# Optimization experiments

Measured on AMD Instinct MI355X. Metric: run time of the kernel, lower is better.

Reference implementation:

```python
import jax, jax.numpy as jnp
import numpy as np
import math

B, S, D = 4, 2048, 1024
H = 16
HD = D // H  # 64
NEG_INF = -1e9


def setup_inputs() -> dict:
    key = jax.random.key(0)
    k1, k2, k3, k4, k5 = jax.random.split(key, 5)
    x = jax.random.normal(k1, (B, S, D), dtype=jnp.float32)
    # rotary frequencies (theta = 10000), shape (S, HD//2)
    inv_freq = 1.0 / (10000.0 ** (jnp.arange(0, HD, 2, dtype=jnp.float32) / HD))
    t = jnp.arange(S, dtype=jnp.float32)
    freqs = jnp.outer(t, inv_freq)  # (S, HD//2)
    freqs_cos = jnp.cos(freqs)
    freqs_sin = jnp.sin(freqs)
    # causal additive mask (1,1,S,S)
    causal = jnp.tril(jnp.ones((S, S), dtype=bool))
    mask = jnp.where(causal, 0.0, NEG_INF).astype(jnp.float32)[None, None]
    scale = 0.02
    wq = jax.random.normal(k2, (D, D), dtype=jnp.float32) * scale
    wk = jax.random.normal(k3, (D, D), dtype=jnp.float32) * scale
    wv = jax.random.normal(k4, (D, D), dtype=jnp.float32) * scale
    wo = jax.random.normal(k5, (D, D), dtype=jnp.float32) * scale
    return {"x": x, "freqs_cos": freqs_cos, "freqs_sin": freqs_sin,
            "mask": mask, "wq": wq, "wk": wk, "wv": wv, "wo": wo}


def _apply_rotary(t, cos, sin):
    # t: (B,S,H,HD); cos/sin: (S, HD//2) broadcast as (1,S,1,HD//2)
    tr = t.reshape(*t.shape[:-1], HD // 2, 2)
    t0, t1 = tr[..., 0], tr[..., 1]
    c = cos[None, :, None, :]
    s = sin[None, :, None, :]
    o0 = t0 * c - t1 * s
    o1 = t0 * s + t1 * c
    return jnp.stack([o0, o1], axis=-1).reshape(t.shape)


def reference(x, freqs_cos, freqs_sin, mask, wq, wk, wv, wo):
    bsz, seqlen, _ = x.shape
    xq = (x @ wq).reshape(bsz, seqlen, H, HD)
    xk = (x @ wk).reshape(bsz, seqlen, H, HD)
    xv = (x @ wv).reshape(bsz, seqlen, H, HD)
    xq = _apply_rotary(xq, freqs_cos, freqs_sin)
    xk = _apply_rotary(xk, freqs_cos, freqs_sin)
    # (B,H,S,HD)
    xq = xq.transpose(0, 2, 1, 3)
    xk = xk.transpose(0, 2, 1, 3)
    xv = xv.transpose(0, 2, 1, 3)
    scores = jnp.einsum('bhqd,bhkd->bhqk', xq, xk) / math.sqrt(HD)
    scores = scores + mask
    probs = jax.nn.softmax(scores.astype(jnp.float32), axis=-1).astype(xq.dtype)
    # dropout is identity in eval mode
    out = jnp.einsum('bhqk,bhkd->bhqd', probs, xv)
    out = out.transpose(0, 2, 1, 3).reshape(bsz, seqlen, H * HD)
    return out @ wo
```

## Files before the change

kernel.cpp:

```cpp
#include <hip/hip_runtime.h>
#include <stdint.h>

typedef short short8 __attribute__((ext_vector_type(8)));
typedef float f32x4 __attribute__((ext_vector_type(4)));
typedef float f32x16 __attribute__((ext_vector_type(16)));
typedef unsigned int u32x4 __attribute__((ext_vector_type(4)));
typedef float float4e __attribute__((ext_vector_type(4)));
typedef unsigned short u16;

#define BB 4
#define SS 2048
#define DD 1024
#define HH 16
#define MM (BB*SS)

__device__ __forceinline__ u16 f2bf(float f) {
    unsigned u = __float_as_uint(f);
    u += 0x7FFFu + ((u >> 16) & 1u);
    return (u16)(u >> 16);
}
__device__ __forceinline__ float bf2f(u16 h) {
    return __uint_as_float(((unsigned)h) << 16);
}
__device__ __forceinline__ unsigned cvtpk(float a, float b) {
    unsigned r;
    asm("v_cvt_pk_bf16_f32 %0, %1, %2" : "=v"(r) : "v"(a), "v"(b));
    return r;
}
__device__ __forceinline__ void gload16(const void* g, void* l) {
    __builtin_amdgcn_global_load_lds(
        (const __attribute__((address_space(1))) unsigned int*)(uintptr_t)g,
        (__attribute__((address_space(3))) unsigned int*)(unsigned)(uintptr_t)l,
        16, 0, 0);
}
__device__ __forceinline__ bool tens_is_bf(const u16* mref) { return mref[1] == 0xCE6Eu; }

__global__ __launch_bounds__(256) void cvt_x(const void* xin, u16* xb, const u16* mref) {
    bool isbf = tens_is_bf(mref);
    size_t i = (size_t)blockIdx.x * 256 + threadIdx.x;
    if (isbf) {
        ((u32x4*)xb)[i] = ((const u32x4*)xin)[i];
    } else {
        const float4e* src = (const float4e*)xin;
        float4e a = src[2*i], b = src[2*i+1];
        u32x4 o;
        o[0] = (unsigned)f2bf(a[0]) | ((unsigned)f2bf(a[1]) << 16);
        o[1] = (unsigned)f2bf(a[2]) | ((unsigned)f2bf(a[3]) << 16);
        o[2] = (unsigned)f2bf(b[0]) | ((unsigned)f2bf(b[1]) << 16);
        o[3] = (unsigned)f2bf(b[2]) | ((unsigned)f2bf(b[3]) << 16);
        ((u32x4*)xb)[i] = o;
    }
}

__global__ __launch_bounds__(256) void trw(const void* w0, const void* w1, const void* w2, const void* w3,
                                           u16* wt, const u16* mref) {
    bool isbf = tens_is_bf(mref);
    const void* w = (blockIdx.z == 0) ? w0 : (blockIdx.z == 1) ? w1 : (blockIdx.z == 2) ? w2 : w3;
    u16* out = wt + (size_t)blockIdx.z * (DD*DD);
    __shared__ float t[32][33];
    int tx = threadIdx.x & 31, ty = threadIdx.x >> 5;
    int n0 = blockIdx.x * 32, k0 = blockIdx.y * 32;
#pragma unroll
    for (int i = 0; i < 4; ++i) {
        int k = k0 + ty*4 + i;
        float v = isbf ? bf2f(((const u16*)w)[(size_t)k*DD + n0 + tx])
                       : ((const float*)w)[(size_t)k*DD + n0 + tx];
        t[ty*4 + i][tx] = v;
    }
    __syncthreads();
#pragma unroll
    for (int i = 0; i < 4; ++i)
        out[(size_t)(n0 + ty*4 + i)*DD + k0 + tx] = f2bf(t[tx][ty*4 + i]);
}

#define QSCALE 0.1803368801111204f
template<int MODE>
__global__ __launch_bounds__(256) void gemm128(const u16* __restrict__ A, const u16* __restrict__ Bt,
                                               u16* outQ, u16* outK, u16* outVT, void* Cout,
                                               const void* fcos, const void* fsin,
                                               const u16* mref) {
    constexpr int SMEMB = (MODE == 1) ? 36864 : 32768;
    __shared__ __align__(16) unsigned char smem[SMEMB];
    int tid = threadIdx.x;
    int w = tid >> 6, l = tid & 63, lo = l & 15, hi = l >> 4;
    int wm = w >> 1, wn = w & 1;
    int wg = blockIdx.x;
    int c = wg & 7, local = wg >> 3;
    int bx = c*8 + (local & 7);
    int by = local >> 3;
    int m0 = bx * 128, n0 = by * 128;

    f32x4 acc[4][4] = {};

    auto stage = [&](int buf, int t) {
        int k0 = t * 32;
#pragma unroll
        for (int i = 0; i < 2; ++i) {
            int o = (i*256 + tid) * 16;
            int row = o >> 6, inb = o & 63;
            int sw  = inb ^ ((row & 3) << 4);
            gload16((const char*)A + ((size_t)(m0 + row)*DD + k0)*2 + sw,
                    smem + buf*16384 + (i*256 + (tid & ~63))*16);
            gload16((const char*)Bt + ((size_t)(n0 + row)*DD + k0)*2 + sw,
                    smem + buf*16384 + 8192 + (i*256 + (tid & ~63))*16);
        }
    };

    stage(0, 0);
    __syncthreads();
    int cur = 0;
    const int NT = DD / 32;
    for (int t = 0; t < NT; ++t) {
        if (t + 1 < NT) stage(cur ^ 1, t + 1);
        const char* Ab = (const char*)(smem + cur*16384);
        const char* Bb = Ab + 8192;
        short8 af[4], bfr[4];
#pragma unroll
        for (int mi = 0; mi < 4; ++mi) {
            int r = wm*64 + mi*16 + lo;
            int ib = hi * 16;
            af[mi] = *(const short8*)(Ab + r*64 + (ib ^ ((r & 3) << 4)));
        }
#pragma unroll
        for (int ni = 0; ni < 4; ++ni) {
            int r = wn*64 + ni*16 + lo;
            int ib = hi * 16;
            bfr[ni] = *(const short8*)(Bb + r*64 + (ib ^ ((r & 3) << 4)));
        }
        __builtin_amdgcn_s_setprio(1);
#pragma unroll
        for (int mi = 0; mi < 4; ++mi)
#pragma unroll
            for (int ni = 0; ni < 4; ++ni)
                acc[mi][ni] = __builtin_amdgcn_mfma_f32_16x16x32_bf16(af[mi], bfr[ni], acc[mi][ni], 0, 0, 0);
        __builtin_amdgcn_s_setprio(0);
        __syncthreads();
        cur ^= 1;
    }

    if (MODE == 1) {
        int wi = n0 >> 10;
        int n0w = n0 & 1023;
        if (wi == 2) {
            __syncthreads();
            u16* vs = (u16*)smem + w * (64*72);
#pragma unroll
            for (int ni = 0; ni < 4; ++ni) {
                int d = ni*16 + lo;
#pragma unroll
                for (int mi = 0; mi < 4; ++mi)
#pragma unroll
                    for (int rr = 0; rr < 2; ++rr) {
                        unsigned pk = (unsigned)f2bf(acc[mi][ni][2*rr]) | ((unsigned)f2bf(acc[mi][ni][2*rr+1]) << 16);
                        *(unsigned*)(vs + d*72 + mi*16 + hi*4 + rr*2) = pk;
                    }
            }
            asm volatile("s_waitcnt lgkmcnt(0)" ::: "memory");
            int bq = (m0 + wm*64) >> 11;
            int s_base = (m0 + wm*64) & (SS-1);
            int h = (n0w + wn*64) >> 6;
#pragma unroll
            for (int p = 0; p < 8; ++p) {
                int idx = p*64 + l;
                int row = idx >> 3, ch = idx & 7;
                short8 vv = *(const short8*)(vs + row*72 + ch*8);
                *(short8*)(outVT + (((size_t)bq*HH + h)*64 + row)*SS + s_base + ch*8) = vv;
            }
        } else {
            bool fbf = (((const u16*)fcos)[0] == 0x3F80u);
            u16* outp = wi ? outK : outQ;
            float oscale = wi ? 1.0f : QSCALE;
#pragma unroll
            for (int mi = 0; mi < 4; ++mi)
#pragma unroll
                for (int ni = 0; ni < 4; ++ni)
#pragma unroll
                    for (int r = 0; r < 4; ++r) {
                        int gm = m0 + wm*64 + mi*16 + hi*4 + r;
                        int gc = n0w + wn*64 + ni*16 + lo;
                        float v  = acc[mi][ni][r];
                        float vp = __shfl_xor(v, 1);
                        int s = gm & (SS-1), d = gc & 63, i2 = d >> 1;
                        float co, sn;
                        if (fbf) { co = bf2f(((const u16*)fcos)[s*32 + i2]); sn = bf2f(((const u16*)fsin)[s*32 + i2]); }
                        else     { co = ((const float*)fcos)[s*32 + i2];     sn = ((const float*)fsin)[s*32 + i2]; }
                        float o = (gc & 1) ? (vp*sn + v*co) : (v*co - vp*sn);
                        o *= oscale;
                        int b = gm >> 11, h = gc >> 6;
                        outp[((((size_t)b*HH + h)*SS + s) << 6) + d] = f2bf(o);
                    }
        }
    } else {
        bool isbf = tens_is_bf(mref);
#pragma unroll
        for (int mi = 0; mi < 4; ++mi)
#pragma unroll
            for (int ni = 0; ni < 4; ++ni)
#pragma unroll
                for (int r = 0; r < 4; ++r) {
                    int gm = m0 + wm*64 + mi*16 + hi*4 + r;
                    int gc = n0 + wn*64 + ni*16 + lo;
                    float v = acc[mi][ni][r];
                    if (isbf) ((u16*)Cout)[(size_t)gm*DD + gc] = f2bf(v);
                    else      ((float*)Cout)[(size_t)gm*DD + gc] = v;
                }
    }
}

__global__ __launch_bounds__(256) void attn(const u16* __restrict__ Q, const u16* __restrict__ K,
                                            const u16* __restrict__ VT, u16* __restrict__ AO) {
    __shared__ __align__(16) u16 Kl[2][64*64];
    __shared__ __align__(16) u16 Vl[2][64*64];
    int bh = blockIdx.x;
    int qt = (gridDim.y - 1) - blockIdx.y;
    int tid = threadIdx.x, w = tid >> 6, l = tid & 63;
    int l31 = l & 31, hi5 = l >> 5;
    const u16* Qb = Q  + (size_t)bh * SS * 64;
    const u16* Kb = K  + (size_t)bh * SS * 64;
    const u16* Vb = VT + (size_t)bh * 64 * SS;
    int q0w = qt*128 + w*32;
    int q   = q0w + l31;

    short8 qf[4];
#pragma unroll
    for (int kc = 0; kc < 4; ++kc)
        qf[kc] = *(const short8*)(Qb + (size_t)q*64 + kc*16 + hi5*8);

    f32x16 oacc[2] = {};
    float m_ = -1e30f, l_ = 0.f;

    auto stage = [&](int buf, int kt) {
        const char* Kt = (const char*)(Kb + (size_t)kt*64*64);
        const char* Vt = (const char*)Vb + (size_t)kt*128;
#pragma unroll
        for (int i = 0; i < 2; ++i) {
            int idx = i*256 + tid;
            int row = idx >> 3, inb = (idx & 7) * 16;
            int sw = inb ^ ((row & 7) << 4);
            gload16(Kt + row*128 + sw,            (char*)Kl[buf] + (i*256 + (tid & ~63))*16);
            gload16(Vt + (size_t)row*(SS*2) + sw, (char*)Vl[buf] + (i*256 + (tid & ~63))*16);
        }
    };

    int nkt = 2*qt + 2;
    stage(0, 0);
    __syncthreads();
    int cur = 0;

    for (int kt = 0; kt < nkt; ++kt) {
        if (kt + 1 < nkt) stage(cur ^ 1, kt + 1);

        if (kt*64 <= q0w + 31) {
            f32x16 sc[2] = {};
            __builtin_amdgcn_s_setprio(1);
#pragma unroll
            for (int kvt = 0; kvt < 2; ++kvt) {
                short8 kf[4];
#pragma unroll
                for (int kc = 0; kc < 4; ++kc) {
                    int row = kvt*32 + l31;
                    int ib = kc*32 + hi5*16;
                    kf[kc] = *(const short8*)((const char*)Kl[cur] + row*128 + (ib ^ ((row & 7) << 4)));
                }
#pragma unroll
                for (int kc = 0; kc < 4; ++kc)
                    sc[kvt] = __builtin_amdgcn_mfma_f32_32x32x16_bf16(kf[kc], qf[kc], sc[kvt], 0, 0, 0);
            }
            __builtin_amdgcn_s_setprio(0);

            if (kt*64 + 63 > q0w) {
#pragma unroll
                for (int kvt = 0; kvt < 2; ++kvt)
#pragma unroll
                    for (int rg = 0; rg < 16; ++rg) {
                        int kv = kt*64 + kvt*32 + (rg & 3) + 8*(rg >> 2) + 4*hi5;
                        if (kv > q) sc[kvt][rg] = -1e9f;
                    }
            }

            float mx = -1e30f;
#pragma unroll
            for (int kvt = 0; kvt < 2; ++kvt)
#pragma unroll
                for (int rg = 0; rg < 16; ++rg) mx = fmaxf(mx, sc[kvt][rg]);
            mx = fmaxf(mx, __shfl_xor(mx, 32));
            if (!__all(mx <= m_ + 8.f)) {
                float mn = fmaxf(m_, mx);
                float al = exp2f(m_ - mn);
                m_ = mn;
                l_ *= al;
#pragma unroll
                for (int dt = 0; dt < 2; ++dt)
#pragma unroll
                    for (int rg = 0; rg < 16; ++rg) oacc[dt][rg] *= al;
            }
            float rs = 0.f;
#pragma unroll
            for (int kvt = 0; kvt < 2; ++kvt)
#pragma unroll
                for (int rg = 0; rg < 16; ++rg) {
                    float p = exp2f(sc[kvt][rg] - m_);
                    sc[kvt][rg] = p;
                    rs += p;
                }
            rs += __shfl_xor(rs, 32);
            l_ += rs;

            short8 pa[4];
#pragma unroll
            for (int kc = 0; kc < 4; ++kc) {
                const int kvt = kc >> 1;
                const int base = (kc & 1) * 8;
                unsigned A0 = cvtpk(sc[kvt][base + 0], sc[kvt][base + 1]);
                unsigned A1 = cvtpk(sc[kvt][base + 2], sc[kvt][base + 3]);
                unsigned B0 = cvtpk(sc[kvt][base + 4], sc[kvt][base + 5]);
                unsigned B1 = cvtpk(sc[kvt][base + 6], sc[kvt][base + 7]);
                asm("v_permlane32_swap_b32 %0, %1" : "+v"(A0), "+v"(B0));
                asm("v_permlane32_swap_b32 %0, %1" : "+v"(A1), "+v"(B1));
                u32x4 pk; pk[0] = A0; pk[1] = A1; pk[2] = B0; pk[3] = B1;
                pa[kc] = __builtin_bit_cast(short8, pk);
            }

            __builtin_amdgcn_s_setprio(1);
#pragma unroll
            for (int dt = 0; dt < 2; ++dt) {
                short8 vf[4];
#pragma unroll
                for (int kc = 0; kc < 4; ++kc) {
                    int row = dt*32 + l31;
                    int ib = kc*32 + hi5*16;
                    vf[kc] = *(const short8*)((const char*)Vl[cur] + row*128 + (ib ^ ((row & 7) << 4)));
                }
#pragma unroll
                for (int kc = 0; kc < 4; ++kc)
                    oacc[dt] = __builtin_amdgcn_mfma_f32_32x32x16_bf16(vf[kc], pa[kc], oacc[dt], 0, 0, 0);
            }
            __builtin_amdgcn_s_setprio(0);
        }

        __syncthreads();
        cur ^= 1;
    }

    int b = bh >> 4, h = bh & 15;
    float inv = 1.0f / l_;
    u16* aor = AO + (size_t)(b*SS + q)*DD + h*64;
#pragma unroll
    for (int dt = 0; dt < 2; ++dt)
#pragma unroll
        for (int j = 0; j < 8; ++j) {
            int r0 = 2*j, r1 = 2*j + 1;
            int d = dt*32 + (r0 & 3) + 8*(r0 >> 2) + 4*hi5;
            unsigned pk = (unsigned)f2bf(oacc[dt][r0] * inv) | ((unsigned)f2bf(oacc[dt][r1] * inv) << 16);
            *(unsigned*)(aor + d) = pk;
        }
}

extern "C" void kernel_launch(void* const* d_in, const int* in_sizes, int n_in,
                              void* d_out, int out_size, void* d_ws, size_t ws_size,
                              hipStream_t stream) {
    const void* x    = d_in[0];
    const void* fcos = d_in[1];
    const void* fsin = d_in[2];
    const u16*  mref = (const u16*)d_in[3];
    const void* wq   = d_in[4];
    const void* wk   = d_in[5];
    const void* wv   = d_in[6];
    const void* wo   = d_in[7];

    u16* ws = (u16*)d_ws;
    const size_t XB = (size_t)MM * DD;
    const size_t WT = (size_t)DD * DD;
    u16* xb  = ws;
    u16* wt  = ws + XB;
    u16* qb  = ws + XB + 4*WT;
    u16* kb  = qb + XB;
    u16* vtb = kb + XB;

    cvt_x<<<4096, 256, 0, stream>>>(x, xb, mref);
    trw<<<dim3(32, 32, 4), 256, 0, stream>>>(wq, wk, wv, wo, wt, mref);
    gemm128<1><<<1536, 256, 0, stream>>>(xb, wt, qb, kb, vtb, nullptr, fcos, fsin, mref);
    attn<<<dim3(64, 16), 256, 0, stream>>>(qb, kb, vtb, xb);
    gemm128<3><<<512, 256, 0, stream>>>(xb, wt + 3*WT, nullptr, nullptr, nullptr, d_out, fcos, fsin, mref);
}
```

Before: 200.5 us.

## Use 2D GEMM grid, precompute LDS offsets, tree-reduce softmax max and sum

The GEMM drops its swizzled 1D block-to-tile remap and switches to a plain 2D grid, which changes L2 locality across workgroups. The attention kernel precomputes the swizzled LDS fragment offsets once per thread instead of recomputing them each iteration. The row max and row sum now use balanced trees instead of serial chains, which shortens dependency latency. Removing the grouped tile ordering may lower cache reuse in the GEMMs.

```diff
diff --git a/kernel.cpp b/kernel.cpp
--- a/kernel.cpp
+++ b/kernel.cpp
@@ -84,11 +84,7 @@
     int tid = threadIdx.x;
     int w = tid >> 6, l = tid & 63, lo = l & 15, hi = l >> 4;
     int wm = w >> 1, wn = w & 1;
-    int wg = blockIdx.x;
-    int c = wg & 7, local = wg >> 3;
-    int bx = c*8 + (local & 7);
-    int by = local >> 3;
-    int m0 = bx * 128, n0 = by * 128;
+    int m0 = blockIdx.x * 128, n0 = blockIdx.y * 128;
 
     f32x4 acc[4][4] = {};
 
@@ -226,6 +222,16 @@
     for (int kc = 0; kc < 4; ++kc)
         qf[kc] = *(const short8*)(Qb + (size_t)q*64 + kc*16 + hi5*8);
 
+    int loff[2][4];
+#pragma unroll
+    for (int g = 0; g < 2; ++g)
+#pragma unroll
+        for (int kc = 0; kc < 4; ++kc) {
+            int row = g*32 + l31;
+            int ib = kc*32 + hi5*16;
+            loff[g][kc] = row*128 + (ib ^ ((row & 7) << 4));
+        }
+
     f32x16 oacc[2] = {};
     float m_ = -1e30f, l_ = 0.f;
 
@@ -251,17 +257,16 @@
         if (kt + 1 < nkt) stage(cur ^ 1, kt + 1);
 
         if (kt*64 <= q0w + 31) {
+            const char* Kc = (const char*)Kl[cur];
+            const char* Vc = (const char*)Vl[cur];
             f32x16 sc[2] = {};
             __builtin_amdgcn_s_setprio(1);
 #pragma unroll
             for (int kvt = 0; kvt < 2; ++kvt) {
                 short8 kf[4];
 #pragma unroll
-                for (int kc = 0; kc < 4; ++kc) {
-                    int row = kvt*32 + l31;
-                    int ib = kc*32 + hi5*16;
-                    kf[kc] = *(const short8*)((const char*)Kl[cur] + row*128 + (ib ^ ((row & 7) << 4)));
-                }
+                for (int kc = 0; kc < 4; ++kc)
+                    kf[kc] = *(const short8*)(Kc + loff[kvt][kc]);
 #pragma unroll
                 for (int kc = 0; kc < 4; ++kc)
                     sc[kvt] = __builtin_amdgcn_mfma_f32_32x32x16_bf16(kf[kc], qf[kc], sc[kvt], 0, 0, 0);
@@ -278,11 +283,12 @@
                     }
             }
 
-            float mx = -1e30f;
-#pragma unroll
-            for (int kvt = 0; kvt < 2; ++kvt)
-#pragma unroll
-                for (int rg = 0; rg < 16; ++rg) mx = fmaxf(mx, sc[kvt][rg]);
+            float m8[8];
+#pragma unroll
+            for (int j = 0; j < 8; ++j)
+                m8[j] = fmaxf(fmaxf(sc[0][j], sc[0][j+8]), fmaxf(sc[1][j], sc[1][j+8]));
+            float mx = fmaxf(fmaxf(fmaxf(m8[0], m8[1]), fmaxf(m8[2], m8[3])),
+                             fmaxf(fmaxf(m8[4], m8[5]), fmaxf(m8[6], m8[7])));
             mx = fmaxf(mx, __shfl_xor(mx, 32));
             if (!__all(mx <= m_ + 8.f)) {
                 float mn = fmaxf(m_, mx);
@@ -294,15 +300,16 @@
 #pragma unroll
                     for (int rg = 0; rg < 16; ++rg) oacc[dt][rg] *= al;
             }
-            float rs = 0.f;
 #pragma unroll
             for (int kvt = 0; kvt < 2; ++kvt)
 #pragma unroll
-                for (int rg = 0; rg < 16; ++rg) {
-                    float p = exp2f(sc[kvt][rg] - m_);
-                    sc[kvt][rg] = p;
-                    rs += p;
-                }
+                for (int rg = 0; rg < 16; ++rg)
+                    sc[kvt][rg] = exp2f(sc[kvt][rg] - m_);
+            float s8[8];
+#pragma unroll
+            for (int j = 0; j < 8; ++j)
+                s8[j] = (sc[0][j] + sc[0][j+8]) + (sc[1][j] + sc[1][j+8]);
+            float rs = ((s8[0] + s8[1]) + (s8[2] + s8[3])) + ((s8[4] + s8[5]) + (s8[6] + s8[7]));
             rs += __shfl_xor(rs, 32);
             l_ += rs;
 
@@ -326,11 +333,8 @@
             for (int dt = 0; dt < 2; ++dt) {
                 short8 vf[4];
 #pragma unroll
-                for (int kc = 0; kc < 4; ++kc) {
-                    int row = dt*32 + l31;
-                    int ib = kc*32 + hi5*16;
-                    vf[kc] = *(const short8*)((const char*)Vl[cur] + row*128 + (ib ^ ((row & 7) << 4)));
-                }
+                for (int kc = 0; kc < 4; ++kc)
+                    vf[kc] = *(const short8*)(Vc + loff[dt][kc]);
 #pragma unroll
                 for (int kc = 0; kc < 4; ++kc)
                     oacc[dt] = __builtin_amdgcn_mfma_f32_32x32x16_bf16(vf[kc], pa[kc], oacc[dt], 0, 0, 0);
@@ -379,7 +383,7 @@
 
     cvt_x<<<4096, 256, 0, stream>>>(x, xb, mref);
     trw<<<dim3(32, 32, 4), 256, 0, stream>>>(wq, wk, wv, wo, wt, mref);
-    gemm128<1><<<1536, 256, 0, stream>>>(xb, wt, qb, kb, vtb, nullptr, fcos, fsin, mref);
+    gemm128<1><<<dim3(64, 24), 256, 0, stream>>>(xb, wt, qb, kb, vtb, nullptr, fcos, fsin, mref);
     attn<<<dim3(64, 16), 256, 0, stream>>>(qb, kb, vtb, xb);
-    gemm128<3><<<512, 256, 0, stream>>>(xb, wt + 3*WT, nullptr, nullptr, nullptr, d_out, fcos, fsin, mref);
-}
+    gemm128<3><<<dim3(64, 8), 256, 0, stream>>>(xb, wt + 3*WT, nullptr, nullptr, nullptr, d_out, fcos, fsin, mref);
+}
```

Measured after the change: 199.8 us. No clear change (-0.3%).
